# Optimization experiments

Measured on AMD Instinct MI355X. Metric: run time of the kernel, lower is better.

Reference implementation:

```python
import jax, jax.numpy as jnp
import numpy as np

BITS = 4            # bits per quantized weight
NPACK = 8           # 32-bit container / 4-bit values
CBITS = 32          # compression dtype bit width (int32)
GROUP = 128         # quantization group size along in_features
IN = 4096
OUT = 11008
BATCH = 32


def _dequant(packed_weight, scale):
    # Unpack signed int4 values: (p << (32 - 4*(e+1))) >> 28, arithmetic shift
    # sign-extends, matching the torch recover() path for weight_dtype=int8.
    e = jnp.arange(NPACK, dtype=jnp.int32)                      # [8]
    shifted = (packed_weight[:, :, None] << (CBITS - BITS * (e + 1))) >> (CBITS - BITS)  # [O, I/8, 8]
    w_int = shifted.reshape(OUT, IN).astype(jnp.int8)           # signed int4 in int8
    # Per-group scale: reshape to [O*I/GROUP, GROUP] * [O*I/GROUP, 1]
    w = w_int.astype(jnp.float32).reshape(-1, GROUP) * scale.reshape(-1, 1)
    return w.reshape(OUT, IN)


def setup_inputs() -> dict:
    key = jax.random.key(0)
    k1, k2, k3, k4 = jax.random.split(key, 4)
    x = jax.random.normal(k1, (BATCH, IN), dtype=jnp.float32)
    packed_weight = jax.random.randint(
        k2, (OUT, IN // NPACK), jnp.iinfo(jnp.int32).min, jnp.iinfo(jnp.int32).max,
        dtype=jnp.int32)
    scale = jax.random.uniform(k3, (OUT, IN // GROUP), dtype=jnp.float32,
                               minval=0.001, maxval=0.02)
    bias = jax.random.normal(k4, (OUT,), dtype=jnp.float32)
    return {"x": x, "packed_weight": packed_weight, "scale": scale, "bias": bias}


def reference(x, packed_weight, scale, bias):
    W = _dequant(packed_weight, scale)      # [OUT, IN] fp32
    return x @ W.T + bias                    # F.linear(x, W, bias)
```

## Files before the change

### kernel.cpp

```cpp
#include <hip/hip_runtime.h>
#include <hip/hip_bf16.h>

#define IN_F   4096
#define OUT_F  11008
#define BATCH  32
#define NG     32
#define PACKS  512

typedef __bf16 bf16x8_t __attribute__((ext_vector_type(8)));
typedef float  floatx4_t __attribute__((ext_vector_type(4)));

__global__ __launch_bounds__(256) void prep_x(const float* __restrict__ x,
                                              unsigned short* __restrict__ xp) {
  int c  = blockIdx.x * 256 + threadIdx.x;
  int mm = c & 31;
  int k0 = ((c >> 5) & 3) * 32 + ((c >> 7) & 3) * 8 + (c >> 9) * 128;
  const float* src = x + mm * IN_F + k0;
  float4 f0 = *(const float4*)(src);
  float4 f1 = *(const float4*)(src + 4);
  float v[8] = {f0.x, f0.y, f0.z, f0.w, f1.x, f1.y, f1.z, f1.w};
  union { unsigned short s[8]; uint4 u; } r;
#pragma unroll
  for (int j = 0; j < 8; ++j) {
    unsigned int u = __float_as_uint(v[j]);
    unsigned int rnd = ((u >> 16) & 1u) + 0x7fffu;
    r.s[j] = (unsigned short)((u + rnd) >> 16);
  }
  *(uint4*)(xp + c * 8) = r.u;
}

__device__ inline bf16x8_t unpack8(int p) {
  union { unsigned short u[8]; bf16x8_t v; } r;
#pragma unroll
  for (int j = 0; j < 8; ++j) {
    int nib = (p << (28 - 4 * j)) >> 28;
    float f = (float)nib;
    r.u[j] = (unsigned short)(__float_as_uint(f) >> 16);
  }
  return r.v;
}

__device__ inline bf16x8_t load_frag(const unsigned short* p) {
  union { uint4 u; bf16x8_t v; } x;
  x.u = *(const uint4*)p;
  return x.v;
}

__global__ __launch_bounds__(256) void wql_main(
    const int* __restrict__ pw, const float* __restrict__ scale,
    const float* __restrict__ bias, const unsigned short* __restrict__ xp,
    float* __restrict__ out) {
  __shared__ float lds[4][BATCH * 32];

  const int tid = threadIdx.x;
  const int l   = tid & 63;
  const int w   = tid >> 6;
  const int col = l & 15;
  const int q   = l >> 4;
  const int n0  = blockIdx.x * 32;
  const int nA  = n0 + col;
  const int nB  = n0 + 16 + col;

  floatx4_t acc00 = {0.f, 0.f, 0.f, 0.f};
  floatx4_t acc01 = {0.f, 0.f, 0.f, 0.f};
  floatx4_t acc10 = {0.f, 0.f, 0.f, 0.f};
  floatx4_t acc11 = {0.f, 0.f, 0.f, 0.f};

  const int g0 = w * 8;
#pragma unroll 1
  for (int gi = 0; gi < 8; ++gi) {
    const int gg = g0 + gi;
    int4 pA = *(const int4*)(pw + nA * PACKS + gg * 16 + q * 4);
    int4 pB = *(const int4*)(pw + nB * PACKS + gg * 16 + q * 4);
    float sA = scale[nA * NG + gg];
    float sB = scale[nB * NG + gg];

    const unsigned short* ab = xp + (gg * 512 + q * 32 + col) * 8;
    bf16x8_t a0[4], a1[4];
#pragma unroll
    for (int t = 0; t < 4; ++t) {
      a0[t] = load_frag(ab + t * 1024);
      a1[t] = load_frag(ab + t * 1024 + 128);
    }

    floatx4_t t00 = {0.f, 0.f, 0.f, 0.f};
    floatx4_t t01 = {0.f, 0.f, 0.f, 0.f};
    floatx4_t t10 = {0.f, 0.f, 0.f, 0.f};
    floatx4_t t11 = {0.f, 0.f, 0.f, 0.f};
    int pAv[4] = {pA.x, pA.y, pA.z, pA.w};
    int pBv[4] = {pB.x, pB.y, pB.z, pB.w};
#pragma unroll
    for (int t = 0; t < 4; ++t) {
      bf16x8_t b0 = unpack8(pAv[t]);
      bf16x8_t b1 = unpack8(pBv[t]);
      t00 = __builtin_amdgcn_mfma_f32_16x16x32_bf16(a0[t], b0, t00, 0, 0, 0);
      t10 = __builtin_amdgcn_mfma_f32_16x16x32_bf16(a1[t], b0, t10, 0, 0, 0);
      t01 = __builtin_amdgcn_mfma_f32_16x16x32_bf16(a0[t], b1, t01, 0, 0, 0);
      t11 = __builtin_amdgcn_mfma_f32_16x16x32_bf16(a1[t], b1, t11, 0, 0, 0);
    }
#pragma unroll
    for (int r = 0; r < 4; ++r) {
      acc00[r] += t00[r] * sA;
      acc10[r] += t10[r] * sA;
      acc01[r] += t01[r] * sB;
      acc11[r] += t11[r] * sB;
    }
  }

#pragma unroll
  for (int r = 0; r < 4; ++r) {
    int row = q * 4 + r;
    lds[w][row * 32 + col]             = acc00[r];
    lds[w][row * 32 + 16 + col]        = acc01[r];
    lds[w][(16 + row) * 32 + col]      = acc10[r];
    lds[w][(16 + row) * 32 + 16 + col] = acc11[r];
  }
  __syncthreads();

  for (int e = tid; e < BATCH * 32; e += 256) {
    int row = e >> 5, cl = e & 31;
    float s = lds[0][e] + lds[1][e] + lds[2][e] + lds[3][e];
    out[row * OUT_F + n0 + cl] = s + bias[n0 + cl];
  }
}

extern "C" void kernel_launch(void* const* d_in, const int* in_sizes, int n_in,
                              void* d_out, int out_size, void* d_ws, size_t ws_size,
                              hipStream_t stream) {
  const float* x     = (const float*)d_in[0];
  const int*   pw    = (const int*)d_in[1];
  const float* scale = (const float*)d_in[2];
  const float* bias  = (const float*)d_in[3];
  float* out = (float*)d_out;
  unsigned short* xp = (unsigned short*)d_ws;

  hipLaunchKernelGGL(prep_x, dim3(16384 / 256), dim3(256), 0, stream, x, xp);
  hipLaunchKernelGGL(wql_main, dim3(OUT_F / 32), dim3(256), 0, stream,
                     pw, scale, bias, xp, out);
}
```

Measured before the change: 84.75 us.

## Split K across eight waves with 16-column tiles, prefetch weights, faster int4 unpack

```diff
diff --git a/kernel.cpp b/kernel.cpp
--- a/kernel.cpp
+++ b/kernel.cpp
@@ -1,5 +1,4 @@
 #include <hip/hip_runtime.h>
-#include <hip/hip_bf16.h>
 
 #define IN_F   4096
 #define OUT_F  11008
@@ -30,97 +29,82 @@
 }
 
 __device__ inline bf16x8_t unpack8(int p) {
-  union { unsigned short u[8]; bf16x8_t v; } r;
+  bf16x8_t r;
 #pragma unroll
   for (int j = 0; j < 8; ++j) {
-    int nib = (p << (28 - 4 * j)) >> 28;
-    float f = (float)nib;
-    r.u[j] = (unsigned short)(__float_as_uint(f) >> 16);
+    unsigned int b = (((unsigned int)p >> (4 * j)) & 0xFu) ^ 0x4B000008u;
+    r[j] = (__bf16)(__uint_as_float(b) - 8388616.0f);
   }
-  return r.v;
+  return r;
 }
 
-__device__ inline bf16x8_t load_frag(const unsigned short* p) {
-  union { uint4 u; bf16x8_t v; } x;
-  x.u = *(const uint4*)p;
-  return x.v;
-}
-
-__global__ __launch_bounds__(256) void wql_main(
+__global__ __launch_bounds__(512, 8) void wql_full(
     const int* __restrict__ pw, const float* __restrict__ scale,
     const float* __restrict__ bias, const unsigned short* __restrict__ xp,
     float* __restrict__ out) {
-  __shared__ float lds[4][BATCH * 32];
+  __shared__ float park[8][BATCH * 16];
 
   const int tid = threadIdx.x;
   const int l   = tid & 63;
   const int w   = tid >> 6;
   const int col = l & 15;
   const int q   = l >> 4;
-  const int n0  = blockIdx.x * 32;
+  const int n0  = blockIdx.x * 16;
   const int nA  = n0 + col;
-  const int nB  = n0 + 16 + col;
 
-  floatx4_t acc00 = {0.f, 0.f, 0.f, 0.f};
-  floatx4_t acc01 = {0.f, 0.f, 0.f, 0.f};
-  floatx4_t acc10 = {0.f, 0.f, 0.f, 0.f};
-  floatx4_t acc11 = {0.f, 0.f, 0.f, 0.f};
+  floatx4_t acc0 = {0.f, 0.f, 0.f, 0.f};
+  floatx4_t acc1 = {0.f, 0.f, 0.f, 0.f};
 
-  const int g0 = w * 8;
+  const int* pwp = pw + nA * PACKS + (w * 4) * 16 + q * 4;
+  int4 pcur = *(const int4*)(pwp);
+
 #pragma unroll 1
-  for (int gi = 0; gi < 8; ++gi) {
-    const int gg = g0 + gi;
-    int4 pA = *(const int4*)(pw + nA * PACKS + gg * 16 + q * 4);
-    int4 pB = *(const int4*)(pw + nB * PACKS + gg * 16 + q * 4);
+  for (int gi = 0; gi < 4; ++gi) {
+    const int gg = w * 4 + gi;
+    int4 pnext;
+    if (gi < 3) pnext = *(const int4*)(pwp + (gi + 1) * 16);
     float sA = scale[nA * NG + gg];
-    float sB = scale[nB * NG + gg];
 
     const unsigned short* ab = xp + (gg * 512 + q * 32 + col) * 8;
     bf16x8_t a0[4], a1[4];
 #pragma unroll
     for (int t = 0; t < 4; ++t) {
-      a0[t] = load_frag(ab + t * 1024);
-      a1[t] = load_frag(ab + t * 1024 + 128);
+      a0[t] = *(const bf16x8_t*)(ab + t * 1024);
+      a1[t] = *(const bf16x8_t*)(ab + t * 1024 + 128);
     }
 
-    floatx4_t t00 = {0.f, 0.f, 0.f, 0.f};
-    floatx4_t t01 = {0.f, 0.f, 0.f, 0.f};
-    floatx4_t t10 = {0.f, 0.f, 0.f, 0.f};
-    floatx4_t t11 = {0.f, 0.f, 0.f, 0.f};
-    int pAv[4] = {pA.x, pA.y, pA.z, pA.w};
-    int pBv[4] = {pB.x, pB.y, pB.z, pB.w};
+    floatx4_t t0 = {0.f, 0.f, 0.f, 0.f};
+    floatx4_t t1 = {0.f, 0.f, 0.f, 0.f};
+    int pv[4] = {pcur.x, pcur.y, pcur.z, pcur.w};
 #pragma unroll
     for (int t = 0; t < 4; ++t) {
-      bf16x8_t b0 = unpack8(pAv[t]);
-      bf16x8_t b1 = unpack8(pBv[t]);
-      t00 = __builtin_amdgcn_mfma_f32_16x16x32_bf16(a0[t], b0, t00, 0, 0, 0);
-      t10 = __builtin_amdgcn_mfma_f32_16x16x32_bf16(a1[t], b0, t10, 0, 0, 0);
-      t01 = __builtin_amdgcn_mfma_f32_16x16x32_bf16(a0[t], b1, t01, 0, 0, 0);
-      t11 = __builtin_amdgcn_mfma_f32_16x16x32_bf16(a1[t], b1, t11, 0, 0, 0);
+      bf16x8_t b = unpack8(pv[t]);
+      t0 = __builtin_amdgcn_mfma_f32_16x16x32_bf16(a0[t], b, t0, 0, 0, 0);
+      t1 = __builtin_amdgcn_mfma_f32_16x16x32_bf16(a1[t], b, t1, 0, 0, 0);
     }
 #pragma unroll
     for (int r = 0; r < 4; ++r) {
-      acc00[r] += t00[r] * sA;
-      acc10[r] += t10[r] * sA;
-      acc01[r] += t01[r] * sB;
-      acc11[r] += t11[r] * sB;
+      acc0[r] += t0[r] * sA;
+      acc1[r] += t1[r] * sA;
     }
+    pcur = pnext;
   }
 
 #pragma unroll
   for (int r = 0; r < 4; ++r) {
     int row = q * 4 + r;
-    lds[w][row * 32 + col]             = acc00[r];
-    lds[w][row * 32 + 16 + col]        = acc01[r];
-    lds[w][(16 + row) * 32 + col]      = acc10[r];
-    lds[w][(16 + row) * 32 + 16 + col] = acc11[r];
+    park[w][row * 16 + col]        = acc0[r];
+    park[w][(16 + row) * 16 + col] = acc1[r];
   }
   __syncthreads();
 
-  for (int e = tid; e < BATCH * 32; e += 256) {
-    int row = e >> 5, cl = e & 31;
-    float s = lds[0][e] + lds[1][e] + lds[2][e] + lds[3][e];
-    out[row * OUT_F + n0 + cl] = s + bias[n0 + cl];
+  {
+    int e = tid;
+    int row = e >> 4, cl = e & 15;
+    float s = park[0][e] + park[1][e] + park[2][e] + park[3][e]
+            + park[4][e] + park[5][e] + park[6][e] + park[7][e]
+            + bias[n0 + cl];
+    out[row * OUT_F + n0 + cl] = s;
   }
 }
 
@@ -135,6 +119,6 @@
   unsigned short* xp = (unsigned short*)d_ws;
 
   hipLaunchKernelGGL(prep_x, dim3(16384 / 256), dim3(256), 0, stream, x, xp);
-  hipLaunchKernelGGL(wql_main, dim3(OUT_F / 32), dim3(256), 0, stream,
+  hipLaunchKernelGGL(wql_full, dim3(OUT_F / 16), dim3(512), 0, stream,
                      pw, scale, bias, xp, out);
 }
```

Result: slower. 86.88 us (+2.5%).
